# Kernel optimization log

Hardware: AMD Instinct MI355X
Metric: run time of the kernel (lower is better)

## Reference

```python
import jax, jax.numpy as jnp
import numpy as np

N_NODES = 65536
DEGREE = 16
N_EDGES = N_NODES * DEGREE
IN_CH = 128
HEADS = 4
OUT_CH = 16
NEG_SLOPE = 0.2


def setup_inputs() -> dict:
    key = jax.random.key(0)
    k1, k2, k3, k4, k5, k6 = jax.random.split(key, 6)
    csr_row_ptr = jnp.arange(N_NODES + 1, dtype=jnp.int64) * DEGREE
    csr_col_ind = jax.random.randint(k1, (N_EDGES,), 0, N_NODES, dtype=jnp.int64)
    sample_count = jnp.ones((N_NODES,), dtype=jnp.int64)
    x_neighboor = jax.random.normal(k2, (N_NODES, IN_CH), dtype=jnp.float32)
    x_target = jax.random.normal(k3, (N_NODES, IN_CH), dtype=jnp.float32)
    # xavier-ish init scales
    W = jax.random.normal(k4, (IN_CH, HEADS * OUT_CH), dtype=jnp.float32) * (2.0 / (IN_CH + HEADS * OUT_CH)) ** 0.5
    attn_l = jax.random.normal(k5, (HEADS, OUT_CH), dtype=jnp.float32) * 0.1
    attn_r = jax.random.normal(k6, (HEADS, OUT_CH), dtype=jnp.float32) * 0.1
    bias = jnp.zeros((HEADS * OUT_CH,), dtype=jnp.float32)
    return {"csr_row_ptr": csr_row_ptr, "csr_col_ind": csr_col_ind,
            "sample_count": sample_count, "x_neighboor": x_neighboor,
            "x_target": x_target, "W": W, "attn_l": attn_l,
            "attn_r": attn_r, "bias": bias}


def reference(csr_row_ptr, csr_col_ind, sample_count, x_neighboor, x_target, W, attn_l, attn_r, bias):
    N = csr_row_ptr.shape[0] - 1
    E = csr_col_ind.shape[0]
    H, C = attn_l.shape
    # linear projection: [Nn, in] @ [in, H*C] -> [Nn, H, C]
    feat = (x_neighboor @ W).reshape(-1, H, C)
    feat_target = feat[:N]
    el = jnp.sum(feat_target * attn_l[None], axis=-1)  # [N, H]
    er = jnp.sum(feat * attn_r[None], axis=-1)         # [Nn, H]
    # row id of each edge from CSR row pointers
    row_id = jnp.searchsorted(csr_row_ptr, jnp.arange(E), side='right') - 1  # [E]
    # spadd_gat: per-edge score = el[row] + er[col], then leaky relu
    w = el[row_id] + er[csr_col_ind]                   # [E, H]
    w = jnp.where(w >= 0, w, NEG_SLOPE * w)
    # segment (per-row) softmax over edges, numerically stable
    wmax = jax.lax.stop_gradient(jax.ops.segment_max(w, row_id, num_segments=N))
    ew = jnp.exp(w - wmax[row_id])
    denom = jax.ops.segment_sum(ew, row_id, num_segments=N)
    alpha = ew / denom[row_id]                         # [E, H]
    # weighted sparse aggregation (gspmm): y[r] = sum_e alpha[e] * feat[col[e]]
    y = jax.ops.segment_sum(alpha[:, :, None] * feat[csr_col_ind], row_id, num_segments=N)  # [N, H, C]
    y = y + bias.reshape(1, H, C)
    return y.reshape(N, H * C)
```

## Files before the change

### kernel.cpp

```cpp
#include <hip/hip_runtime.h>
#include <hip/hip_bf16.h>

#define IN_CH 128
#define HC 64
#define NEG_SLOPE 0.2f

__device__ __forceinline__ float bf2f(unsigned short u) {
    union { unsigned int i; float f; } v; v.i = ((unsigned int)u) << 16; return v.f;
}
__device__ __forceinline__ void unpack2(unsigned int u, float& a, float& b) {
    union { unsigned int i; float f; } lo, hi;
    lo.i = u << 16; hi.i = u & 0xffff0000u;
    a = lo.f; b = hi.f;
}

__device__ __forceinline__ bool detect_f32(const void* p) {
    const unsigned int* w = (const unsigned int*)p;
    int cnt = 0;
    #pragma unroll
    for (int i = 0; i < 64; ++i) {
        unsigned short lo = (unsigned short)(w[i] & 0xffffu);
        int ex = (lo >> 7) & 0xff;
        if (lo == 0 || (ex >= 100 && ex <= 150)) ++cnt;
    }
    return cnt < 48;
}

__global__ __launch_bounds__(256, 2) void feat_gemm_kernel(
    const void* __restrict__ xv_,
    const void* __restrict__ Wv_,
    const void* __restrict__ attn_l_,
    const void* __restrict__ attn_r_,
    float* __restrict__ feat,
    float* __restrict__ el,
    float* __restrict__ er,
    int N)
{
    __shared__ float xsT[IN_CH * 64];
    __shared__ float Wsf[IN_CH * HC];
    const int tid = threadIdx.x;
    const int row0 = blockIdx.x * 64;
    const int wv = tid >> 6, lane = tid & 63;

    const bool f32 = detect_f32(xv_);

    if (f32) {
        const float* Wf = (const float*)Wv_;
        for (int i = tid; i < IN_CH * HC / 4; i += 256) {
            float4 v = *(const float4*)(Wf + i * 4);
            Wsf[i*4+0] = v.x; Wsf[i*4+1] = v.y; Wsf[i*4+2] = v.z; Wsf[i*4+3] = v.w;
        }
        const float* xf = (const float*)xv_;
        for (int it = 0; it < 4; ++it) {
            int kg = (wv * 4 + it) * 8;
            const float* src = xf + (size_t)(row0 + lane) * IN_CH + kg;
            float4 a = *(const float4*)src;
            float4 b = *(const float4*)(src + 4);
            xsT[(kg+0)*64 + lane] = a.x;
            xsT[(kg+1)*64 + lane] = a.y;
            xsT[(kg+2)*64 + lane] = a.z;
            xsT[(kg+3)*64 + lane] = a.w;
            xsT[(kg+4)*64 + lane] = b.x;
            xsT[(kg+5)*64 + lane] = b.y;
            xsT[(kg+6)*64 + lane] = b.z;
            xsT[(kg+7)*64 + lane] = b.w;
        }
    } else {
        const uint4* W4 = (const uint4*)Wv_;
        for (int i = tid; i < IN_CH * HC / 8; i += 256) {
            uint4 u = W4[i];
            float f0,f1,f2,f3,f4,f5,f6,f7;
            unpack2(u.x,f0,f1); unpack2(u.y,f2,f3); unpack2(u.z,f4,f5); unpack2(u.w,f6,f7);
            int b = i * 8;
            Wsf[b+0]=f0; Wsf[b+1]=f1; Wsf[b+2]=f2; Wsf[b+3]=f3;
            Wsf[b+4]=f4; Wsf[b+5]=f5; Wsf[b+6]=f6; Wsf[b+7]=f7;
        }
        const unsigned short* x = (const unsigned short*)xv_;
        for (int it = 0; it < 4; ++it) {
            int kg = (wv * 4 + it) * 8;
            uint4 u = *(const uint4*)(x + (size_t)(row0 + lane) * IN_CH + kg);
            float f0,f1,f2,f3,f4,f5,f6,f7;
            unpack2(u.x,f0,f1); unpack2(u.y,f2,f3); unpack2(u.z,f4,f5); unpack2(u.w,f6,f7);
            xsT[(kg+0)*64 + lane] = f0;
            xsT[(kg+1)*64 + lane] = f1;
            xsT[(kg+2)*64 + lane] = f2;
            xsT[(kg+3)*64 + lane] = f3;
            xsT[(kg+4)*64 + lane] = f4;
            xsT[(kg+5)*64 + lane] = f5;
            xsT[(kg+6)*64 + lane] = f6;
            xsT[(kg+7)*64 + lane] = f7;
        }
    }
    __syncthreads();

    const int r0 = (tid & 15) * 4;
    const int c0 = (tid >> 4) * 4;
    float acc[4][4] = {};
    #pragma unroll 8
    for (int k = 0; k < IN_CH; ++k) {
        float4 xvv = *(const float4*)&xsT[k * 64 + r0];
        float4 wvv = *(const float4*)&Wsf[k * HC + c0];
        acc[0][0] += xvv.x * wvv.x; acc[0][1] += xvv.x * wvv.y;
        acc[0][2] += xvv.x * wvv.z; acc[0][3] += xvv.x * wvv.w;
        acc[1][0] += xvv.y * wvv.x; acc[1][1] += xvv.y * wvv.y;
        acc[1][2] += xvv.y * wvv.z; acc[1][3] += xvv.y * wvv.w;
        acc[2][0] += xvv.z * wvv.x; acc[2][1] += xvv.z * wvv.y;
        acc[2][2] += xvv.z * wvv.z; acc[2][3] += xvv.z * wvv.w;
        acc[3][0] += xvv.w * wvv.x; acc[3][1] += xvv.w * wvv.y;
        acc[3][2] += xvv.w * wvv.z; acc[3][3] += xvv.w * wvv.w;
    }

    #pragma unroll
    for (int i = 0; i < 4; ++i) {
        int row = row0 + r0 + i;
        float4 v = make_float4(acc[i][0], acc[i][1], acc[i][2], acc[i][3]);
        *(float4*)&feat[(size_t)row * HC + c0] = v;
    }

    float alv[4], arv[4];
    if (f32) {
        const float* alf = (const float*)attn_l_;
        const float* arf = (const float*)attn_r_;
        #pragma unroll
        for (int j = 0; j < 4; ++j) { alv[j] = alf[c0 + j]; arv[j] = arf[c0 + j]; }
    } else {
        const unsigned short* al = (const unsigned short*)attn_l_;
        const unsigned short* ar = (const unsigned short*)attn_r_;
        #pragma unroll
        for (int j = 0; j < 4; ++j) { alv[j] = bf2f(al[c0 + j]); arv[j] = bf2f(ar[c0 + j]); }
    }
    const int h = wv;
    #pragma unroll
    for (int i = 0; i < 4; ++i) {
        float pl = 0.f, pr = 0.f;
        #pragma unroll
        for (int j = 0; j < 4; ++j) { pl += acc[i][j] * alv[j]; pr += acc[i][j] * arv[j]; }
        pl += __shfl_xor(pl, 16, 64); pl += __shfl_xor(pl, 32, 64);
        pr += __shfl_xor(pr, 16, 64); pr += __shfl_xor(pr, 32, 64);
        if (((tid >> 4) & 3) == 0) {
            int row = row0 + r0 + i;
            el[row * 4 + h] = pl;
            er[row * 4 + h] = pr;
        }
    }
}

__global__ __launch_bounds__(256) void gat_aggregate_kernel(
    const int* __restrict__ row_ptr32,
    const int* __restrict__ col_ind32,
    const float* __restrict__ feat,
    const float* __restrict__ el,
    const float* __restrict__ er,
    const float* __restrict__ bias,
    float* __restrict__ out,
    int N)
{
    const int lane = threadIdx.x & 63;
    const int node = blockIdx.x * 4 + (threadIdx.x >> 6);
    if (node >= N) return;

    const bool idx64 = (row_ptr32[1] != 16);
    int start, deg;
    if (idx64) {
        start = row_ptr32[2 * node];
        deg   = row_ptr32[2 * node + 2] - start;
    } else {
        start = row_ptr32[node];
        deg   = row_ptr32[node + 1] - start;
    }

    const int e = lane & 15;
    const int h = lane >> 4;
    int colv = 0;
    if (lane < 16 && lane < deg) {
        int ei = start + lane;
        colv = idx64 ? col_ind32[2 * ei] : col_ind32[ei];
    }
    int cole = __shfl(colv, e, 64);

    float w;
    if (e < deg) {
        float ww = el[node * 4 + h] + er[(size_t)cole * 4 + h];
        w = (ww >= 0.f) ? ww : NEG_SLOPE * ww;
    } else {
        w = -INFINITY;
    }
    float m = w;
    #pragma unroll
    for (int o = 8; o >= 1; o >>= 1) m = fmaxf(m, __shfl_xor(m, o, 16));
    float ew = (e < deg) ? __expf(w - m) : 0.f;
    float s = ew;
    #pragma unroll
    for (int o = 8; o >= 1; o >>= 1) s += __shfl_xor(s, o, 16);
    float alpha = (s > 0.f) ? (ew / s) : 0.f;

    float acc = 0.f;
    #pragma unroll
    for (int e2 = 0; e2 < 16; ++e2) {
        int c2 = __shfl(colv, e2, 64);
        float a = __shfl(alpha, (lane & 48) + e2, 64);
        acc += a * feat[(size_t)c2 * HC + lane];
    }
    acc += bias[lane];
    out[(size_t)node * HC + lane] = acc;
}

extern "C" void kernel_launch(void* const* d_in, const int* in_sizes, int n_in,
                              void* d_out, int out_size, void* d_ws, size_t ws_size,
                              hipStream_t stream) {
    const int* row_ptr      = (const int*)d_in[0];
    const int* col_ind      = (const int*)d_in[1];
    const void* x           = d_in[3];
    const void* W           = d_in[5];
    const void* attn_l      = d_in[6];
    const void* attn_r      = d_in[7];
    const float* bias       = (const float*)d_in[8];

    const int N = out_size / HC;

    float* feat = (float*)d_ws;
    float* el   = feat + (size_t)N * HC;
    float* er   = el + (size_t)N * 4;

    feat_gemm_kernel<<<N / 64, 256, 0, stream>>>(x, W, attn_l, attn_r, feat, el, er, N);
    gat_aggregate_kernel<<<(N + 3) / 4, 256, 0, stream>>>(row_ptr, col_ind, feat, el, er, bias,
                                                          (float*)d_out, N);
}
```

Before: 172.0 us.

## Use bf16 MFMA for feature projection GEMM with fragment-packed LDS layout

Replaces the scalar fp32 FMA GEMM in the projection kernel with MFMA 16x16x32 bf16 instructions. x and W are converted from fp32 to bf16 with round-to-nearest-even and stored in shared memory already packed in MFMA fragment order. The attention dot products become shuffle reductions over the accumulator layout. The fp32/bf16 input-type detection is dropped, which shrinks shared memory and lets more blocks run per CU, but bf16 rounding of the inputs lowers precision.

```diff
diff --git a/kernel.cpp b/kernel.cpp
--- a/kernel.cpp
+++ b/kernel.cpp
@@ -5,142 +5,112 @@
 #define HC 64
 #define NEG_SLOPE 0.2f
 
-__device__ __forceinline__ float bf2f(unsigned short u) {
-    union { unsigned int i; float f; } v; v.i = ((unsigned int)u) << 16; return v.f;
-}
-__device__ __forceinline__ void unpack2(unsigned int u, float& a, float& b) {
-    union { unsigned int i; float f; } lo, hi;
-    lo.i = u << 16; hi.i = u & 0xffff0000u;
-    a = lo.f; b = hi.f;
+typedef __attribute__((ext_vector_type(8))) short short8;
+typedef __attribute__((ext_vector_type(4))) float floatx4;
+
+__device__ __forceinline__ unsigned short f2bf_rne(float f) {
+    unsigned int u = __float_as_uint(f);
+    u += 0x7fffu + ((u >> 16) & 1u);
+    return (unsigned short)(u >> 16);
 }
 
-__device__ __forceinline__ bool detect_f32(const void* p) {
-    const unsigned int* w = (const unsigned int*)p;
-    int cnt = 0;
-    #pragma unroll
-    for (int i = 0; i < 64; ++i) {
-        unsigned short lo = (unsigned short)(w[i] & 0xffffu);
-        int ex = (lo >> 7) & 0xff;
-        if (lo == 0 || (ex >= 100 && ex <= 150)) ++cnt;
-    }
-    return cnt < 48;
-}
-
-__global__ __launch_bounds__(256, 2) void feat_gemm_kernel(
-    const void* __restrict__ xv_,
-    const void* __restrict__ Wv_,
-    const void* __restrict__ attn_l_,
-    const void* __restrict__ attn_r_,
+__global__ __launch_bounds__(256, 4) void feat_gemm_kernel(
+    const float* __restrict__ xf,
+    const float* __restrict__ Wf,
+    const float* __restrict__ attn_l,
+    const float* __restrict__ attn_r,
     float* __restrict__ feat,
     float* __restrict__ el,
     float* __restrict__ er,
     int N)
 {
-    __shared__ float xsT[IN_CH * 64];
-    __shared__ float Wsf[IN_CH * HC];
+    __shared__ unsigned short xb[64 * IN_CH];
+    __shared__ unsigned short wb[IN_CH * HC];
     const int tid = threadIdx.x;
     const int row0 = blockIdx.x * 64;
-    const int wv = tid >> 6, lane = tid & 63;
 
-    const bool f32 = detect_f32(xv_);
-
-    if (f32) {
-        const float* Wf = (const float*)Wv_;
-        for (int i = tid; i < IN_CH * HC / 4; i += 256) {
-            float4 v = *(const float4*)(Wf + i * 4);
-            Wsf[i*4+0] = v.x; Wsf[i*4+1] = v.y; Wsf[i*4+2] = v.z; Wsf[i*4+3] = v.w;
+    {
+        const int row = tid >> 2;
+        const int t   = row >> 4;
+        const int mp  = row & 15;
+        const int c   = tid & 3;
+        const float4* src = (const float4*)(xf + (size_t)(row0 + row) * IN_CH + c * 32);
+        #pragma unroll
+        for (int i = 0; i < 8; ++i) {
+            float4 v = src[i];
+            const int q  = i >> 1;
+            const int j0 = (i & 1) * 4;
+            const int lane = q * 16 + mp;
+            unsigned int p0 = (unsigned int)f2bf_rne(v.x) | ((unsigned int)f2bf_rne(v.y) << 16);
+            unsigned int p1 = (unsigned int)f2bf_rne(v.z) | ((unsigned int)f2bf_rne(v.w) << 16);
+            uint2 pk = make_uint2(p0, p1);
+            *(uint2*)&xb[(((t * 4 + c) * 64 + lane) * 8) + j0] = pk;
         }
-        const float* xf = (const float*)xv_;
-        for (int it = 0; it < 4; ++it) {
-            int kg = (wv * 4 + it) * 8;
-            const float* src = xf + (size_t)(row0 + lane) * IN_CH + kg;
-            float4 a = *(const float4*)src;
-            float4 b = *(const float4*)(src + 4);
-            xsT[(kg+0)*64 + lane] = a.x;
-            xsT[(kg+1)*64 + lane] = a.y;
-            xsT[(kg+2)*64 + lane] = a.z;
-            xsT[(kg+3)*64 + lane] = a.w;
-            xsT[(kg+4)*64 + lane] = b.x;
-            xsT[(kg+5)*64 + lane] = b.y;
-            xsT[(kg+6)*64 + lane] = b.z;
-            xsT[(kg+7)*64 + lane] = b.w;
-        }
-    } else {
-        const uint4* W4 = (const uint4*)Wv_;
-        for (int i = tid; i < IN_CH * HC / 8; i += 256) {
-            uint4 u = W4[i];
-            float f0,f1,f2,f3,f4,f5,f6,f7;
-            unpack2(u.x,f0,f1); unpack2(u.y,f2,f3); unpack2(u.z,f4,f5); unpack2(u.w,f6,f7);
-            int b = i * 8;
-            Wsf[b+0]=f0; Wsf[b+1]=f1; Wsf[b+2]=f2; Wsf[b+3]=f3;
-            Wsf[b+4]=f4; Wsf[b+5]=f5; Wsf[b+6]=f6; Wsf[b+7]=f7;
-        }
-        const unsigned short* x = (const unsigned short*)xv_;
-        for (int it = 0; it < 4; ++it) {
-            int kg = (wv * 4 + it) * 8;
-            uint4 u = *(const uint4*)(x + (size_t)(row0 + lane) * IN_CH + kg);
-            float f0,f1,f2,f3,f4,f5,f6,f7;
-            unpack2(u.x,f0,f1); unpack2(u.y,f2,f3); unpack2(u.z,f4,f5); unpack2(u.w,f6,f7);
-            xsT[(kg+0)*64 + lane] = f0;
-            xsT[(kg+1)*64 + lane] = f1;
-            xsT[(kg+2)*64 + lane] = f2;
-            xsT[(kg+3)*64 + lane] = f3;
-            xsT[(kg+4)*64 + lane] = f4;
-            xsT[(kg+5)*64 + lane] = f5;
-            xsT[(kg+6)*64 + lane] = f6;
-            xsT[(kg+7)*64 + lane] = f7;
+    }
+    {
+        const float4* W4 = (const float4*)Wf;
+        #pragma unroll
+        for (int i = 0; i < 8; ++i) {
+            int fi = tid + 256 * i;
+            float4 v = W4[fi];
+            int k  = fi >> 4;
+            int n0 = (fi & 15) * 4;
+            int c  = k >> 5;
+            int q  = (k & 31) >> 3;
+            int j  = k & 7;
+            int ct  = n0 >> 4;
+            int np0 = n0 & 15;
+            float e[4] = {v.x, v.y, v.z, v.w};
+            #pragma unroll
+            for (int t2 = 0; t2 < 4; ++t2) {
+                int lane = q * 16 + (np0 + t2);
+                wb[(((ct * 4 + c) * 64 + lane) * 8) + j] = f2bf_rne(e[t2]);
+            }
         }
     }
     __syncthreads();
 
-    const int r0 = (tid & 15) * 4;
-    const int c0 = (tid >> 4) * 4;
-    float acc[4][4] = {};
-    #pragma unroll 8
-    for (int k = 0; k < IN_CH; ++k) {
-        float4 xvv = *(const float4*)&xsT[k * 64 + r0];
-        float4 wvv = *(const float4*)&Wsf[k * HC + c0];
-        acc[0][0] += xvv.x * wvv.x; acc[0][1] += xvv.x * wvv.y;
-        acc[0][2] += xvv.x * wvv.z; acc[0][3] += xvv.x * wvv.w;
-        acc[1][0] += xvv.y * wvv.x; acc[1][1] += xvv.y * wvv.y;
-        acc[1][2] += xvv.y * wvv.z; acc[1][3] += xvv.y * wvv.w;
-        acc[2][0] += xvv.z * wvv.x; acc[2][1] += xvv.z * wvv.y;
-        acc[2][2] += xvv.z * wvv.z; acc[2][3] += xvv.z * wvv.w;
-        acc[3][0] += xvv.w * wvv.x; acc[3][1] += xvv.w * wvv.y;
-        acc[3][2] += xvv.w * wvv.z; acc[3][3] += xvv.w * wvv.w;
+    const int w   = tid >> 6;
+    const int lane = tid & 63;
+
+    floatx4 acc[4];
+    #pragma unroll
+    for (int ct = 0; ct < 4; ++ct) acc[ct] = (floatx4){0.f, 0.f, 0.f, 0.f};
+
+    #pragma unroll
+    for (int c = 0; c < 4; ++c) {
+        short8 afrag = *(const short8*)&xb[((w * 4 + c) * 64 + lane) * 8];
+        #pragma unroll
+        for (int ct = 0; ct < 4; ++ct) {
+            short8 bfrag = *(const short8*)&wb[((ct * 4 + c) * 64 + lane) * 8];
+            acc[ct] = __builtin_amdgcn_mfma_f32_16x16x32_bf16(afrag, bfrag, acc[ct], 0, 0, 0);
+        }
     }
 
+    const int q  = lane >> 4;
+    const int np = lane & 15;
+    float al[4], ar[4];
     #pragma unroll
-    for (int i = 0; i < 4; ++i) {
-        int row = row0 + r0 + i;
-        float4 v = make_float4(acc[i][0], acc[i][1], acc[i][2], acc[i][3]);
-        *(float4*)&feat[(size_t)row * HC + c0] = v;
-    }
+    for (int h = 0; h < 4; ++h) { al[h] = attn_l[h * 16 + np]; ar[h] = attn_r[h * 16 + np]; }
 
-    float alv[4], arv[4];
-    if (f32) {
-        const float* alf = (const float*)attn_l_;
-        const float* arf = (const float*)attn_r_;
+    #pragma unroll
+    for (int ct = 0; ct < 4; ++ct) {
         #pragma unroll
-        for (int j = 0; j < 4; ++j) { alv[j] = alf[c0 + j]; arv[j] = arf[c0 + j]; }
-    } else {
-        const unsigned short* al = (const unsigned short*)attn_l_;
-        const unsigned short* ar = (const unsigned short*)attn_r_;
-        #pragma unroll
-        for (int j = 0; j < 4; ++j) { alv[j] = bf2f(al[c0 + j]); arv[j] = bf2f(ar[c0 + j]); }
-    }
-    const int h = wv;
-    #pragma unroll
-    for (int i = 0; i < 4; ++i) {
-        float pl = 0.f, pr = 0.f;
-        #pragma unroll
-        for (int j = 0; j < 4; ++j) { pl += acc[i][j] * alv[j]; pr += acc[i][j] * arv[j]; }
-        pl += __shfl_xor(pl, 16, 64); pl += __shfl_xor(pl, 32, 64);
-        pr += __shfl_xor(pr, 16, 64); pr += __shfl_xor(pr, 32, 64);
-        if (((tid >> 4) & 3) == 0) {
-            int row = row0 + r0 + i;
-            el[row * 4 + h] = pl;
-            er[row * 4 + h] = pr;
+        for (int r = 0; r < 4; ++r) {
+            int row = row0 + w * 16 + q * 4 + r;
+            float v = acc[ct][r];
+            feat[(size_t)row * HC + ct * 16 + np] = v;
+            float pl = v * al[ct];
+            float pr = v * ar[ct];
+            #pragma unroll
+            for (int o = 8; o >= 1; o >>= 1) {
+                pl += __shfl_xor(pl, o, 16);
+                pr += __shfl_xor(pr, o, 16);
+            }
+            if (np == 0) {
+                el[row * 4 + ct] = pl;
+                er[row * 4 + ct] = pr;
+            }
         }
     }
 }
@@ -210,10 +180,10 @@
                               hipStream_t stream) {
     const int* row_ptr      = (const int*)d_in[0];
     const int* col_ind      = (const int*)d_in[1];
-    const void* x           = d_in[3];
-    const void* W           = d_in[5];
-    const void* attn_l      = d_in[6];
-    const void* attn_r      = d_in[7];
+    const float* x          = (const float*)d_in[3];
+    const float* W          = (const float*)d_in[5];
+    const float* attn_l     = (const float*)d_in[6];
+    const float* attn_r     = (const float*)d_in[7];
     const float* bias       = (const float*)d_in[8];
 
     const int N = out_size / HC;
```

Result: faster. 160.1 us (-6.9%).
